# Performance work log

Hardware: AMD Instinct MI355X
Metric: run time of the kernel (lower is better)

## Reference

```python
import jax, jax.numpy as jnp
import numpy as np

B, D, H, DM, O = 8192, 512, 1024, 2048, 256


def setup_inputs() -> dict:
    key = jax.random.key(0)
    ks = jax.random.split(key, 24)
    def rn(k, shape, scale=1.0):
        return jax.random.normal(k, shape, dtype=jnp.float32) * scale
    w = 0.02  # weight init scale
    return {
        "x":  rn(ks[0], (B, D)),
        "h0": rn(ks[1], (B, H), 0.1), "h1": rn(ks[2], (B, H), 0.1),
        "c0": rn(ks[3], (B, H), 0.1), "c1": rn(ks[4], (B, H), 0.1),
        # Bernoulli keep masks with model_prob=1.0 -> all ones
        "m0": jnp.ones((B, H), jnp.float32), "m1": jnp.ones((B, H), jnp.float32),
        # layer 0 gate weights: in = D + H = 1536
        "Wf0": rn(ks[5], (D + H, H), w), "bf0": jnp.full((H,), 0.01, jnp.float32),
        "Wi0": rn(ks[6], (D + H, H), w), "bi0": jnp.full((H,), 0.01, jnp.float32),
        "Wc0": rn(ks[7], (D + H, H), w), "bc0": jnp.full((H,), 0.01, jnp.float32),
        "Wo0": rn(ks[8], (D + H, H), w), "bo0": jnp.full((H,), 0.01, jnp.float32),
        # layer 1 gate weights: in = H + H = 2048
        "Wf1": rn(ks[9],  (2 * H, H), w), "bf1": jnp.full((H,), 0.01, jnp.float32),
        "Wi1": rn(ks[10], (2 * H, H), w), "bi1": jnp.full((H,), 0.01, jnp.float32),
        "Wc1": rn(ks[11], (2 * H, H), w), "bc1": jnp.full((H,), 0.01, jnp.float32),
        "Wo1": rn(ks[12], (2 * H, H), w), "bo1": jnp.full((H,), 0.01, jnp.float32),
        # output MLP: H -> DM -> O (identity activation per default nn.Sequential())
        "Wm1": rn(ks[13], (H, DM), w), "bm1": jnp.full((DM,), 0.01, jnp.float32),
        "Wm2": rn(ks[14], (DM, O), w), "bm2": jnp.full((O,), 0.01, jnp.float32),
    }


def _lstm_cell(comb, c, Wf, bf, Wi, bi, Wc, bc, Wo, bo):
    # fuse the 4 gate GEMMs into one matmul, then split
    W = jnp.concatenate([Wf, Wi, Wc, Wo], axis=1)      # [in, 4H]
    b = jnp.concatenate([bf, bi, bc, bo])               # [4H]
    g = comb @ W + b                                    # [B, 4H]
    f, i, ct, o = jnp.split(g, 4, axis=1)
    c_new = jax.nn.sigmoid(f) * c + jax.nn.sigmoid(i) * jnp.tanh(ct)
    h_new = jax.nn.sigmoid(o) * jnp.tanh(c_new)
    return h_new, c_new


def reference(x, h0, h1, c0, c1, m0, m1,
              Wf0, bf0, Wi0, bi0, Wc0, bc0, Wo0, bo0,
              Wf1, bf1, Wi1, bi1, Wc1, bc1, Wo1, bo1,
              Wm1, bm1, Wm2, bm2):
    # layer 0: combined = cat(input, h0 * mask0)
    comb0 = jnp.concatenate([x, h0 * m0], axis=1)       # [B, D+H]
    h0n, c0n = _lstm_cell(comb0, c0, Wf0, bf0, Wi0, bi0, Wc0, bc0, Wo0, bo0)
    # layer 1: combined = cat(h0_new * mask0, h1 * mask1)
    comb1 = jnp.concatenate([h0n * m0, h1 * m1], axis=1)  # [B, 2H]
    h1n, c1n = _lstm_cell(comb1, c1, Wf1, bf1, Wi1, bi1, Wc1, bc1, Wo1, bo1)
    # output MLP (dropout p=0 is identity; activation is identity Sequential)
    out = (h1n @ Wm1 + bm1) @ Wm2 + bm2                 # [B, O]
    return out, h0n, h1n, c0n, c1n
```

## Files before the change

### kernel.cpp

```cpp
#include <hip/hip_runtime.h>
#include <hip/hip_bf16.h>
#include <cstdint>
#include <cstddef>

#define DI __device__ __forceinline__

typedef __attribute__((ext_vector_type(8))) short short8;
typedef __attribute__((ext_vector_type(4))) float f32x4;

static constexpr int Bb = 8192, Dd = 512, Hh = 1024;

DI short f2b(float f) {
  union { __hip_bfloat16 h; short s; } u;
  u.h = __float2bfloat16(f);
  return u.s;
}

DI float sigm(float x) {
  float e = __builtin_amdgcn_exp2f(-1.4426950408889634f * x);
  return __builtin_amdgcn_rcpf(1.0f + e);
}
DI float tanh_(float x) {
  float xc = fminf(fmaxf(x, -20.0f), 20.0f);
  float e = __builtin_amdgcn_exp2f(-2.8853900817779268f * xc);
  return (1.0f - e) * __builtin_amdgcn_rcpf(1.0f + e);
}

DI void gload16(const void* g, void* l) {
  __builtin_amdgcn_global_load_lds(
      (const __attribute__((address_space(1))) uint32_t*)g,
      (__attribute__((address_space(3))) uint32_t*)l, 16, 0, 0);
}


__global__ void conv_A0(const float* __restrict__ x, const float* __restrict__ h0,
                        const float* __restrict__ m0, short* __restrict__ A0) {
  const int row = blockIdx.x, t = threadIdx.x;
  float v[8];
  if (t < 64) {
    const float4* p = (const float4*)(x + (size_t)row * Dd + t * 8);
    float4 a = p[0], b = p[1];
    v[0] = a.x; v[1] = a.y; v[2] = a.z; v[3] = a.w;
    v[4] = b.x; v[5] = b.y; v[6] = b.z; v[7] = b.w;
  } else {
    const int j = t * 8 - 512;
    const float4* ph = (const float4*)(h0 + (size_t)row * Hh + j);
    const float4* pm = (const float4*)(m0 + (size_t)row * Hh + j);
    float4 a = ph[0], b = ph[1], ma = pm[0], mb = pm[1];
    v[0] = a.x * ma.x; v[1] = a.y * ma.y; v[2] = a.z * ma.z; v[3] = a.w * ma.w;
    v[4] = b.x * mb.x; v[5] = b.y * mb.y; v[6] = b.z * mb.z; v[7] = b.w * mb.w;
  }
  short8 o;
  #pragma unroll
  for (int q = 0; q < 8; q++) o[q] = f2b(v[q]);
  *(short8*)(A0 + (size_t)row * 1536 + t * 8) = o;
}

__global__ void conv_A1hi(const float* __restrict__ h1, const float* __restrict__ m1,
                          short* __restrict__ A1) {
  const int row = blockIdx.x, t = threadIdx.x;
  const int j = t * 8;
  const float4* ph = (const float4*)(h1 + (size_t)row * Hh + j);
  const float4* pm = (const float4*)(m1 + (size_t)row * Hh + j);
  float4 a = ph[0], b = ph[1], ma = pm[0], mb = pm[1];
  float v[8] = {a.x * ma.x, a.y * ma.y, a.z * ma.z, a.w * ma.w,
                b.x * mb.x, b.y * mb.y, b.z * mb.z, b.w * mb.w};
  short8 o;
  #pragma unroll
  for (int q = 0; q < 8; q++) o[q] = f2b(v[q]);
  *(short8*)(A1 + (size_t)row * 2048 + 1024 + j) = o;
}

__global__ void transpose_conv4(const float* __restrict__ s0, const float* __restrict__ s1,
                                const float* __restrict__ s2, const float* __restrict__ s3,
                                short* __restrict__ dst, int N, int K) {
  __shared__ float t[64][65];
  const int g = blockIdx.z;
  const float* src = (g == 0) ? s0 : (g == 1) ? s1 : (g == 2) ? s2 : s3;
  const int k0 = blockIdx.x * 64, n0 = blockIdx.y * 64;
  const int tid = threadIdx.x;
  const int r = tid >> 2, c0 = (tid & 3) * 16;
  const float* s = src + (size_t)(k0 + r) * N + n0 + c0;
  #pragma unroll
  for (int q = 0; q < 16; q += 4) {
    float4 v = *(const float4*)(s + q);
    t[r][c0 + q + 0] = v.x; t[r][c0 + q + 1] = v.y;
    t[r][c0 + q + 2] = v.z; t[r][c0 + q + 3] = v.w;
  }
  __syncthreads();
  const int n = n0 + r;
  const int j = (n >> 4) * 64 + g * 16 + (n & 15);
  short8 o0, o1;
  #pragma unroll
  for (int q = 0; q < 8; q++) o0[q] = f2b(t[c0 + q][r]);
  #pragma unroll
  for (int q = 0; q < 8; q++) o1[q] = f2b(t[c0 + 8 + q][r]);
  short* d = dst + (size_t)j * K + k0 + c0;
  *(short8*)d = o0;
  *((short8*)d + 1) = o1;
}

__global__ void transpose_conv(const float* __restrict__ src, short* __restrict__ dst,
                               int N, int K) {
  __shared__ float t[64][65];
  const int k0 = blockIdx.x * 64, n0 = blockIdx.y * 64;
  const int tid = threadIdx.x;
  const int r = tid >> 2, c0 = (tid & 3) * 16;
  const float* s = src + (size_t)(k0 + r) * N + n0 + c0;
  #pragma unroll
  for (int q = 0; q < 16; q += 4) {
    float4 v = *(const float4*)(s + q);
    t[r][c0 + q + 0] = v.x; t[r][c0 + q + 1] = v.y;
    t[r][c0 + q + 2] = v.z; t[r][c0 + q + 3] = v.w;
  }
  __syncthreads();
  const int n = n0 + r;
  short8 o0, o1;
  #pragma unroll
  for (int q = 0; q < 8; q++) o0[q] = f2b(t[c0 + q][r]);
  #pragma unroll
  for (int q = 0; q < 8; q++) o1[q] = f2b(t[c0 + 8 + q][r]);
  short* d = dst + (size_t)n * K + k0 + c0;
  *(short8*)d = o0;
  *((short8*)d + 1) = o1;
}

__global__ void conv_plain(const float* __restrict__ src, short* __restrict__ dst, int n8) {
  const int id = blockIdx.x * blockDim.x + threadIdx.x;
  if (id >= n8) return;
  const float4* p = (const float4*)(src + (size_t)id * 8);
  float4 a = p[0], b = p[1];
  short8 o;
  o[0] = f2b(a.x); o[1] = f2b(a.y); o[2] = f2b(a.z); o[3] = f2b(a.w);
  o[4] = f2b(b.x); o[5] = f2b(b.y); o[6] = f2b(b.z); o[7] = f2b(b.w);
  *(short8*)(dst + (size_t)id * 8) = o;
}

__global__ void bp_init(const float* __restrict__ bm2, float* __restrict__ bp) {
  bp[threadIdx.x] = bm2[threadIdx.x];
}
__global__ void bp_acc(const float* __restrict__ bm1, const float* __restrict__ Wm2,
                       float* __restrict__ bp) {
  const int o = threadIdx.x;
  const int k0 = blockIdx.x * 64;
  float s = 0.f;
  #pragma unroll 4
  for (int k = 0; k < 64; k++) s += bm1[k0 + k] * Wm2[(size_t)(k0 + k) * 256 + o];
  atomicAdd(&bp[o], s);
}

template <int EPI>
__global__ __launch_bounds__(256) void gemm_bt(
    const short* __restrict__ A, const short* __restrict__ Bt, int K,
    short* __restrict__ Cb, int ldc,
    float* __restrict__ outp, const float* __restrict__ bpv) {
  __shared__ __align__(16) short sA[128 * 32];
  __shared__ __align__(16) short sB[128 * 32];
  const int tid = threadIdx.x;
  const int lane = tid & 63;
  const int wave = tid >> 6;
  const int wm = wave >> 1, wn = wave & 1;
  const int bm = blockIdx.x, bn = blockIdx.y;
  const int lr = lane & 15, lq = lane >> 4;

  f32x4 acc[4][4] = {};

  const short* pA = A + ((size_t)(bm * 128 + (tid >> 2))) * K + (tid & 3) * 8;
  const short* pB = Bt + ((size_t)(bn * 128 + (tid >> 2))) * K + (tid & 3) * 8;
  short* lA = sA + tid * 8;
  short* lB = sB + tid * 8;
  const int aoff = (wm * 64 + lr) * 32 + lq * 8;
  const int boff = (wn * 64 + lr) * 32 + lq * 8;

  for (int k0 = 0; k0 < K; k0 += 32) {
    gload16(pA + k0, lA);
    gload16(pA + (size_t)64 * K + k0, lA + 2048);
    gload16(pB + k0, lB);
    gload16(pB + (size_t)64 * K + k0, lB + 2048);
    __syncthreads();
    short8 af[4], bv[4];
    #pragma unroll
    for (int m = 0; m < 4; m++) af[m] = *(const short8*)&sA[aoff + m * 512];
    #pragma unroll
    for (int n = 0; n < 4; n++) bv[n] = *(const short8*)&sB[boff + n * 512];
    #pragma unroll
    for (int m = 0; m < 4; m++)
      #pragma unroll
      for (int n = 0; n < 4; n++)
        acc[m][n] = __builtin_amdgcn_mfma_f32_16x16x32_bf16(af[m], bv[n], acc[m][n], 0, 0, 0);
    __syncthreads();
  }

  const int crow0 = bm * 128 + wm * 64 + lq * 4;
  const int ccol0 = bn * 128 + wn * 64 + lr;

  if constexpr (EPI == 0) {
    #pragma unroll
    for (int m = 0; m < 4; m++)
      #pragma unroll
      for (int r = 0; r < 4; r++) {
        const int row = crow0 + m * 16 + r;
        #pragma unroll
        for (int n = 0; n < 4; n++)
          Cb[(size_t)row * ldc + ccol0 + n * 16] = f2b(acc[m][n][r]);
      }
  } else {
    float bvv[4];
    #pragma unroll
    for (int n = 0; n < 4; n++) bvv[n] = bpv[ccol0 + n * 16];
    #pragma unroll
    for (int m = 0; m < 4; m++)
      #pragma unroll
      for (int r = 0; r < 4; r++) {
        const int row = crow0 + m * 16 + r;
        #pragma unroll
        for (int n = 0; n < 4; n++)
          outp[(size_t)row * 256 + ccol0 + n * 16] = acc[m][n][r] + bvv[n];
      }
  }
}


#define STA(buf, h, kt) { const short* s_ = gA + (size_t)(h) * 64 * K + (size_t)(kt) * 64; \
    gload16(s_ + aS0, &sA[buf][h][tid * 8]);                                               \
    gload16(s_ + aS1, &sA[buf][h][4096 + tid * 8]); }
#define STB(buf, h, kt) { const short* s_ = gB + (size_t)(h) * 128 * K + (size_t)(kt) * 64; \
    gload16(s_ + bS0, &sB[buf][h][tid * 8]);                                                \
    gload16(s_ + bS1, &sB[buf][h][4096 + tid * 8]); }

#define LDB(buf) {                                                \
    const short* bb = &sB[buf][bh][brb];                          \
    _Pragma("unroll") for (int n = 0; n < 4; n++) {               \
      bv[n][0] = *(const short8*)(bb + n * 1024 + sw0);           \
      bv[n][1] = *(const short8*)(bb + n * 1024 + sw1); } }

#define LDA_(buf, q, av) {                                        \
    const short* ab = &sA[buf][(q) >> 1][arb + ((q) & 1) * 2048]; \
    av[0][0] = *(const short8*)(ab + sw0);                        \
    av[0][1] = *(const short8*)(ab + sw1);                        \
    av[1][0] = *(const short8*)(ab + 1024 + sw0);                 \
    av[1][1] = *(const short8*)(ab + 1024 + sw1); }

#define MM(q, av) {                                               \
    __builtin_amdgcn_s_setprio(1);                                \
    _Pragma("unroll") for (int m = 0; m < 2; m++)                 \
    _Pragma("unroll") for (int n = 0; n < 4; n++) {               \
      acc[2*(q)+m][n] = __builtin_amdgcn_mfma_f32_16x16x32_bf16(av[m][0], bv[n][0], acc[2*(q)+m][n], 0, 0, 0); \
      acc[2*(q)+m][n] = __builtin_amdgcn_mfma_f32_16x16x32_bf16(av[m][1], bv[n][1], acc[2*(q)+m][n], 0, 0, 0); } \
    __builtin_amdgcn_s_setprio(0); }

#define BAR() asm volatile("s_barrier" ::: "memory")
#define VM6() asm volatile("s_waitcnt vmcnt(6)" ::: "memory")

#define PH(buf, q, STG, vm) { short8 av[2][2]; LDA_(buf, q, av); STG; \
    if (vm) VM6(); BAR(); MM(q, av); BAR(); }

__global__ __launch_bounds__(512, 2) void gemm8_lstm(
    const short* __restrict__ A, const short* __restrict__ Bt, const int K,
    const float* __restrict__ cprev, float* __restrict__ hout,
    float* __restrict__ cout, short* __restrict__ anext, const int ldan,
    const float* __restrict__ mask,
    const float* __restrict__ bF, const float* __restrict__ bI,
    const float* __restrict__ bC, const float* __restrict__ bO) {
  __shared__ __align__(16) short sA[2][2][8192];
  __shared__ __align__(16) short sB[2][2][8192];
  const int tid = threadIdx.x;
  const int lane = tid & 63, wid = tid >> 6;
  const int wr = wid >> 2, wc = wid & 3;
  const int lr = lane & 15, lq = lane >> 4;

  const int bm = blockIdx.x, bn = blockIdx.y;

  const int NT = K >> 6;
  const int NIT = NT >> 1;

  const int r0 = tid >> 3;
  const int csw = (tid & 7) ^ (r0 & 7);
  const int growA0 = ((r0 >> 5) & 1) * 32 + (r0 & 31);
  const int growA1 = 128 + growA0;
  const size_t aS0 = (size_t)growA0 * K + csw * 8;
  const size_t aS1 = (size_t)growA1 * K + csw * 8;
  const size_t bS0 = (size_t)r0 * K + csw * 8;
  const size_t bS1 = (size_t)(r0 + 64) * K + csw * 8;
  const short* gA = A + (size_t)bm * 256 * K;
  const short* gB = Bt + (size_t)bn * 256 * K;

  const int arb = (wr * 64 + lr) * 64;
  const int brb = ((wc & 1) * 64 + lr) * 64;
  const int bh = wc >> 1;
  const int sw0 = ((lq) ^ (lr & 7)) * 8;
  const int sw1 = ((4 + lq) ^ (lr & 7)) * 8;

  f32x4 acc[8][4] = {};
  short8 bv[4][2];

  STB(0, 0, 0); STB(0, 1, 0); STA(0, 0, 0); STA(0, 1, 0);
  STB(1, 0, 1); STB(1, 1, 1); STA(1, 0, 1);
  VM6(); BAR();

  for (int it = 0; it < NIT; ++it) {
    const int k1 = 2 * it + 1;
    int t2 = 2 * it + 2; if (t2 >= NT) t2 = 0;
    int t3 = 2 * it + 3; if (t3 >= NT) t3 = 1;
    { short8 av[2][2]; LDB(0); LDA_(0, 0, av); STA(1, 1, k1); BAR(); MM(0, av); BAR(); }
    PH(0, 1, STB(0, 0, t2), 0);
    PH(0, 2, STB(0, 1, t2), 0);
    PH(0, 3, STA(0, 0, t2), 1);
    { short8 av[2][2]; LDB(1); LDA_(1, 0, av); STA(0, 1, t2); BAR(); MM(0, av); BAR(); }
    PH(1, 1, STB(1, 0, t3), 0);
    PH(1, 2, STB(1, 1, t3), 0);
    PH(1, 3, STA(1, 0, t3), 1);
  }

  const int n = (bn * 4 + wc) * 16 + lr;
  const float bf_ = bF[n], bi_ = bI[n], bc_ = bC[n], bo_ = bO[n];
  const int row0 = bm * 256 + wr * 128 + lq * 4;

  float cp[4], mk[4], cpn[4], mkn[4];
  #pragma unroll
  for (int rr = 0; rr < 4; rr++) {
    const size_t idx = (size_t)(row0 + rr) * 1024 + n;
    cp[rr] = cprev[idx];
    mk[rr] = mask ? mask[idx] : 1.0f;
  }
  #pragma unroll
  for (int mf = 0; mf < 8; mf++) {
    if (mf < 7) {
      #pragma unroll
      for (int rr = 0; rr < 4; rr++) {
        const size_t idx2 = (size_t)(row0 + (mf + 1) * 16 + rr) * 1024 + n;
        cpn[rr] = cprev[idx2];
        mkn[rr] = mask ? mask[idx2] : 1.0f;
      }
    }
    #pragma unroll
    for (int rr = 0; rr < 4; rr++) {
      const int row = row0 + mf * 16 + rr;
      const size_t idx = (size_t)row * 1024 + n;
      const float fg = sigm(acc[mf][0][rr] + bf_);
      const float ig = sigm(acc[mf][1][rr] + bi_);
      const float cg = tanh_(acc[mf][2][rr] + bc_);
      const float og = sigm(acc[mf][3][rr] + bo_);
      const float cn = fg * cp[rr] + ig * cg;
      const float hn = og * tanh_(cn);
      cout[idx] = cn;
      hout[idx] = hn;
      anext[(size_t)row * ldan + n] = f2b(hn * mk[rr]);
    }
    #pragma unroll
    for (int rr = 0; rr < 4; rr++) { cp[rr] = cpn[rr]; mk[rr] = mkn[rr]; }
  }
}


extern "C" void kernel_launch(void* const* d_in, const int* in_sizes, int n_in,
                              void* d_out, int out_size, void* d_ws, size_t ws_size,
                              hipStream_t stream) {
  (void)in_sizes; (void)n_in; (void)out_size; (void)ws_size;
  const float* x   = (const float*)d_in[0];
  const float* h0  = (const float*)d_in[1];
  const float* h1  = (const float*)d_in[2];
  const float* c0  = (const float*)d_in[3];
  const float* c1  = (const float*)d_in[4];
  const float* m0  = (const float*)d_in[5];
  const float* m1  = (const float*)d_in[6];
  const float* Wf0 = (const float*)d_in[7];  const float* bf0 = (const float*)d_in[8];
  const float* Wi0 = (const float*)d_in[9];  const float* bi0 = (const float*)d_in[10];
  const float* Wc0 = (const float*)d_in[11]; const float* bc0 = (const float*)d_in[12];
  const float* Wo0 = (const float*)d_in[13]; const float* bo0 = (const float*)d_in[14];
  const float* Wf1 = (const float*)d_in[15]; const float* bf1 = (const float*)d_in[16];
  const float* Wi1 = (const float*)d_in[17]; const float* bi1 = (const float*)d_in[18];
  const float* Wc1 = (const float*)d_in[19]; const float* bc1 = (const float*)d_in[20];
  const float* Wo1 = (const float*)d_in[21]; const float* bo1 = (const float*)d_in[22];
  const float* Wm1 = (const float*)d_in[23]; const float* bm1 = (const float*)d_in[24];
  const float* Wm2 = (const float*)d_in[25]; const float* bm2 = (const float*)d_in[26];

  float* dout  = (float*)d_out;
  float* out_o = dout;
  float* h0n   = dout + 2097152;
  float* h1n   = h0n + 8388608;
  float* c0n   = h1n + 8388608;
  float* c1n   = c0n + 8388608;

  char* ws = (char*)d_ws;
  short* A0   = (short*)(ws);
  short* A1   = (short*)(ws + 25165824);
  short* A2   = (short*)(ws + 58720256);
  short* WT0  = (short*)(ws + 75497472);
  short* WT1  = (short*)(ws + 88080384);
  short* Wm1b = (short*)(ws + 104857600);
  short* Wm2T = (short*)(ws + 109051904);
  short* WpT  = (short*)(ws + 110100480);
  float* bp   = (float*)(ws + 110624768);

  conv_A0<<<dim3(8192), dim3(192), 0, stream>>>(x, h0, m0, A0);
  conv_A1hi<<<dim3(8192), dim3(128), 0, stream>>>(h1, m1, A1);
  transpose_conv4<<<dim3(24, 16, 4), dim3(256), 0, stream>>>(Wf0, Wi0, Wc0, Wo0, WT0, 1024, 1536);
  transpose_conv4<<<dim3(32, 16, 4), dim3(256), 0, stream>>>(Wf1, Wi1, Wc1, Wo1, WT1, 1024, 2048);
  conv_plain<<<dim3(1024), dim3(256), 0, stream>>>(Wm1, Wm1b, 262144);
  transpose_conv<<<dim3(32, 4), dim3(256), 0, stream>>>(Wm2, Wm2T, 256, 2048);
  bp_init<<<dim3(1), dim3(256), 0, stream>>>(bm2, bp);
  bp_acc<<<dim3(32), dim3(256), 0, stream>>>(bm1, Wm2, bp);

  gemm_bt<0><<<dim3(2, 8), dim3(256), 0, stream>>>(
      Wm2T, Wm1b, 2048, WpT, 1024, nullptr, nullptr);

  gemm8_lstm<<<dim3(32, 16), dim3(512), 0, stream>>>(
      A0, WT0, 1536, c0, h0n, c0n, A1, 2048, m0, bf0, bi0, bc0, bo0);

  gemm8_lstm<<<dim3(32, 16), dim3(512), 0, stream>>>(
      A1, WT1, 2048, c1, h1n, c1n, A2, 1024, nullptr, bf1, bi1, bc1, bo1);

  gemm_bt<1><<<dim3(64, 2), dim3(256), 0, stream>>>(
      A2, WpT, 1024, nullptr, 0, out_o, bp);
}
```

Before: 392.5 us.

## Shrink LSTM GEMM tile from 256x256 to 128x128 with more blocks

Replaces the 256x256 output tile per 512-thread block with a 128x128 tile. The grid grows from 32x16 to 64x32, LDS per block is halved, and launch bounds ask for 4 blocks per CU instead of 2. The warp layout changes to 4x2 with 2x4 MFMA fragments per wave, and the prefetch schedule is simplified to fit. The aim is higher occupancy and more parallel blocks to hide latency, at the cost of lower arithmetic intensity and more global/L2 traffic per FLOP.

```diff
diff --git a/kernel.cpp b/kernel.cpp
--- a/kernel.cpp
+++ b/kernel.cpp
@@ -221,54 +221,45 @@
 }
 
 
-#define STA(buf, h, kt) { const short* s_ = gA + (size_t)(h) * 64 * K + (size_t)(kt) * 64; \
-    gload16(s_ + aS0, &sA[buf][h][tid * 8]);                                               \
-    gload16(s_ + aS1, &sA[buf][h][4096 + tid * 8]); }
-#define STB(buf, h, kt) { const short* s_ = gB + (size_t)(h) * 128 * K + (size_t)(kt) * 64; \
-    gload16(s_ + bS0, &sB[buf][h][tid * 8]);                                                \
-    gload16(s_ + bS1, &sB[buf][h][4096 + tid * 8]); }
+#define STA(buf, h, kt) gload16(gA + (size_t)(h) * 64 * K + (size_t)(kt) * 64 + rofs, \
+                                &sA[buf][h][tid * 8])
+#define STB(buf, h, kt) gload16(gB + (size_t)(h) * 64 * K + (size_t)(kt) * 64 + rofs, \
+                                &sB[buf][h][tid * 8])
 
 #define LDB(buf) {                                                \
-    const short* bb = &sB[buf][bh][brb];                          \
+    const short* bb = &sB[buf][wn][lr * 64];                      \
     _Pragma("unroll") for (int n = 0; n < 4; n++) {               \
       bv[n][0] = *(const short8*)(bb + n * 1024 + sw0);           \
       bv[n][1] = *(const short8*)(bb + n * 1024 + sw1); } }
 
-#define LDA_(buf, q, av) {                                        \
-    const short* ab = &sA[buf][(q) >> 1][arb + ((q) & 1) * 2048]; \
-    av[0][0] = *(const short8*)(ab + sw0);                        \
-    av[0][1] = *(const short8*)(ab + sw1);                        \
-    av[1][0] = *(const short8*)(ab + 1024 + sw0);                 \
-    av[1][1] = *(const short8*)(ab + 1024 + sw1); }
-
-#define MM(q, av) {                                               \
+#define LDA_(buf, mf, av) {                                       \
+    const short* ab = &sA[buf][wm >> 1][((wm & 1) * 32 + (mf) * 16 + lr) * 64]; \
+    av[0] = *(const short8*)(ab + sw0);                           \
+    av[1] = *(const short8*)(ab + sw1); }
+
+#define MM(mf, av) {                                              \
     __builtin_amdgcn_s_setprio(1);                                \
-    _Pragma("unroll") for (int m = 0; m < 2; m++)                 \
     _Pragma("unroll") for (int n = 0; n < 4; n++) {               \
-      acc[2*(q)+m][n] = __builtin_amdgcn_mfma_f32_16x16x32_bf16(av[m][0], bv[n][0], acc[2*(q)+m][n], 0, 0, 0); \
-      acc[2*(q)+m][n] = __builtin_amdgcn_mfma_f32_16x16x32_bf16(av[m][1], bv[n][1], acc[2*(q)+m][n], 0, 0, 0); } \
+      acc[mf][n] = __builtin_amdgcn_mfma_f32_16x16x32_bf16(av[0], bv[n][0], acc[mf][n], 0, 0, 0); \
+      acc[mf][n] = __builtin_amdgcn_mfma_f32_16x16x32_bf16(av[1], bv[n][1], acc[mf][n], 0, 0, 0); } \
     __builtin_amdgcn_s_setprio(0); }
 
 #define BAR() asm volatile("s_barrier" ::: "memory")
-#define VM6() asm volatile("s_waitcnt vmcnt(6)" ::: "memory")
-
-#define PH(buf, q, STG, vm) { short8 av[2][2]; LDA_(buf, q, av); STG; \
-    if (vm) VM6(); BAR(); MM(q, av); BAR(); }
-
-__global__ __launch_bounds__(512, 2) void gemm8_lstm(
+#define VM2() asm volatile("s_waitcnt vmcnt(2)" ::: "memory")
+
+__global__ __launch_bounds__(512, 4) void gemm4_lstm(
     const short* __restrict__ A, const short* __restrict__ Bt, const int K,
     const float* __restrict__ cprev, float* __restrict__ hout,
     float* __restrict__ cout, short* __restrict__ anext, const int ldan,
     const float* __restrict__ mask,
     const float* __restrict__ bF, const float* __restrict__ bI,
     const float* __restrict__ bC, const float* __restrict__ bO) {
-  __shared__ __align__(16) short sA[2][2][8192];
-  __shared__ __align__(16) short sB[2][2][8192];
+  __shared__ __align__(16) short sA[2][2][4096];
+  __shared__ __align__(16) short sB[2][2][4096];
   const int tid = threadIdx.x;
   const int lane = tid & 63, wid = tid >> 6;
-  const int wr = wid >> 2, wc = wid & 3;
+  const int wm = wid >> 1, wn = wid & 1;
   const int lr = lane & 15, lq = lane >> 4;
-
   const int bm = blockIdx.x, bn = blockIdx.y;
 
   const int NT = K >> 6;
@@ -276,63 +267,49 @@
 
   const int r0 = tid >> 3;
   const int csw = (tid & 7) ^ (r0 & 7);
-  const int growA0 = ((r0 >> 5) & 1) * 32 + (r0 & 31);
-  const int growA1 = 128 + growA0;
-  const size_t aS0 = (size_t)growA0 * K + csw * 8;
-  const size_t aS1 = (size_t)growA1 * K + csw * 8;
-  const size_t bS0 = (size_t)r0 * K + csw * 8;
-  const size_t bS1 = (size_t)(r0 + 64) * K + csw * 8;
-  const short* gA = A + (size_t)bm * 256 * K;
-  const short* gB = Bt + (size_t)bn * 256 * K;
-
-  const int arb = (wr * 64 + lr) * 64;
-  const int brb = ((wc & 1) * 64 + lr) * 64;
-  const int bh = wc >> 1;
+  const size_t rofs = (size_t)r0 * K + csw * 8;
+  const short* gA = A + (size_t)bm * 128 * K;
+  const short* gB = Bt + (size_t)bn * 128 * K;
+
   const int sw0 = ((lq) ^ (lr & 7)) * 8;
   const int sw1 = ((4 + lq) ^ (lr & 7)) * 8;
 
-  f32x4 acc[8][4] = {};
+  f32x4 acc[2][4] = {};
   short8 bv[4][2];
 
   STB(0, 0, 0); STB(0, 1, 0); STA(0, 0, 0); STA(0, 1, 0);
-  STB(1, 0, 1); STB(1, 1, 1); STA(1, 0, 1);
-  VM6(); BAR();
+  STB(1, 0, 1); STB(1, 1, 1);
+  VM2(); BAR();
 
   for (int it = 0; it < NIT; ++it) {
     const int k1 = 2 * it + 1;
     int t2 = 2 * it + 2; if (t2 >= NT) t2 = 0;
     int t3 = 2 * it + 3; if (t3 >= NT) t3 = 1;
-    { short8 av[2][2]; LDB(0); LDA_(0, 0, av); STA(1, 1, k1); BAR(); MM(0, av); BAR(); }
-    PH(0, 1, STB(0, 0, t2), 0);
-    PH(0, 2, STB(0, 1, t2), 0);
-    PH(0, 3, STA(0, 0, t2), 1);
-    { short8 av[2][2]; LDB(1); LDA_(1, 0, av); STA(0, 1, t2); BAR(); MM(0, av); BAR(); }
-    PH(1, 1, STB(1, 0, t3), 0);
-    PH(1, 2, STB(1, 1, t3), 0);
-    PH(1, 3, STA(1, 0, t3), 1);
-  }
-
-  const int n = (bn * 4 + wc) * 16 + lr;
+    { short8 av[2]; LDB(0); LDA_(0, 0, av); STA(1, 0, k1); STA(1, 1, k1);
+      BAR(); MM(0, av); BAR(); }
+    { short8 av[2]; LDA_(0, 1, av); STB(0, 0, t2); STB(0, 1, t2);
+      VM2(); BAR(); MM(1, av); BAR(); }
+    { short8 av[2]; LDB(1); LDA_(1, 0, av); STA(0, 0, t2); STA(0, 1, t2);
+      BAR(); MM(0, av); BAR(); }
+    { short8 av[2]; LDA_(1, 1, av); STB(1, 0, t3); STB(1, 1, t3);
+      VM2(); BAR(); MM(1, av); BAR(); }
+  }
+
+  const int n = bn * 32 + wn * 16 + lr;
   const float bf_ = bF[n], bi_ = bI[n], bc_ = bC[n], bo_ = bO[n];
-  const int row0 = bm * 256 + wr * 128 + lq * 4;
-
-  float cp[4], mk[4], cpn[4], mkn[4];
-  #pragma unroll
-  for (int rr = 0; rr < 4; rr++) {
-    const size_t idx = (size_t)(row0 + rr) * 1024 + n;
-    cp[rr] = cprev[idx];
-    mk[rr] = mask ? mask[idx] : 1.0f;
-  }
-  #pragma unroll
-  for (int mf = 0; mf < 8; mf++) {
-    if (mf < 7) {
-      #pragma unroll
-      for (int rr = 0; rr < 4; rr++) {
-        const size_t idx2 = (size_t)(row0 + (mf + 1) * 16 + rr) * 1024 + n;
-        cpn[rr] = cprev[idx2];
-        mkn[rr] = mask ? mask[idx2] : 1.0f;
-      }
+  const int row0 = bm * 128 + wm * 32 + lq * 4;
+
+  float cp[2][4], mk[2][4];
+  #pragma unroll
+  for (int mf = 0; mf < 2; mf++)
+    #pragma unroll
+    for (int rr = 0; rr < 4; rr++) {
+      const size_t idx = (size_t)(row0 + mf * 16 + rr) * 1024 + n;
+      cp[mf][rr] = cprev[idx];
+      mk[mf][rr] = mask ? mask[idx] : 1.0f;
     }
+  #pragma unroll
+  for (int mf = 0; mf < 2; mf++) {
     #pragma unroll
     for (int rr = 0; rr < 4; rr++) {
       const int row = row0 + mf * 16 + rr;
@@ -341,14 +318,12 @@
       const float ig = sigm(acc[mf][1][rr] + bi_);
       const float cg = tanh_(acc[mf][2][rr] + bc_);
       const float og = sigm(acc[mf][3][rr] + bo_);
-      const float cn = fg * cp[rr] + ig * cg;
+      const float cn = fg * cp[mf][rr] + ig * cg;
       const float hn = og * tanh_(cn);
       cout[idx] = cn;
       hout[idx] = hn;
-      anext[(size_t)row * ldan + n] = f2b(hn * mk[rr]);
+      anext[(size_t)row * ldan + n] = f2b(hn * mk[mf][rr]);
     }
-    #pragma unroll
-    for (int rr = 0; rr < 4; rr++) { cp[rr] = cpn[rr]; mk[rr] = mkn[rr]; }
   }
 }
 
@@ -405,10 +380,10 @@
   gemm_bt<0><<<dim3(2, 8), dim3(256), 0, stream>>>(
       Wm2T, Wm1b, 2048, WpT, 1024, nullptr, nullptr);
 
-  gemm8_lstm<<<dim3(32, 16), dim3(512), 0, stream>>>(
+  gemm4_lstm<<<dim3(64, 32), dim3(512), 0, stream>>>(
       A0, WT0, 1536, c0, h0n, c0n, A1, 2048, m0, bf0, bi0, bc0, bo0);
 
-  gemm8_lstm<<<dim3(32, 16), dim3(512), 0, stream>>>(
+  gemm4_lstm<<<dim3(64, 32), dim3(512), 0, stream>>>(
       A1, WT1, 2048, c1, h1n, c1n, A2, 1024, nullptr, bf1, bi1, bc1, bo1);
 
   gemm_bt<1><<<dim3(64, 2), dim3(256), 0, stream>>>(
```

New measurement: 405.1 us. +3.2%, slower.

## Split LSTM gate GEMM across 16 waves per block instead of 8

Applied to the files above, without the earlier changes.

Reworks the fused LSTM gate GEMM kernel to launch 1024 threads (16 waves) per 256x256 tile instead of 512. Each wave now owns 64 rows instead of 128, so it holds half the accumulators, and the global-to-LDS staging needs one 16-byte load per thread per half-tile. The wait count, the per-wave A-fragment addressing and the epilogue row mapping are changed to match. The aim is more latency hiding and lower register pressure per wave, at the cost of more barrier participants and B-fragment LDS reads repeated across twice as many waves.

```diff
diff --git a/kernel.cpp b/kernel.cpp
--- a/kernel.cpp
+++ b/kernel.cpp
@@ -221,41 +221,33 @@
 }
 
 
-#define STA(buf, h, kt) { const short* s_ = gA + (size_t)(h) * 64 * K + (size_t)(kt) * 64; \
-    gload16(s_ + aS0, &sA[buf][h][tid * 8]);                                               \
-    gload16(s_ + aS1, &sA[buf][h][4096 + tid * 8]); }
-#define STB(buf, h, kt) { const short* s_ = gB + (size_t)(h) * 128 * K + (size_t)(kt) * 64; \
-    gload16(s_ + bS0, &sB[buf][h][tid * 8]);                                                \
-    gload16(s_ + bS1, &sB[buf][h][4096 + tid * 8]); }
+#define STA(buf, h, kt) gload16(gA + (size_t)(h) * 128 * K + (size_t)(kt) * 64 + rofs, \
+                                &sA[buf][h][tid * 8])
+#define STB(buf, h, kt) gload16(gB + (size_t)(h) * 128 * K + (size_t)(kt) * 64 + rofs, \
+                                &sB[buf][h][tid * 8])
 
 #define LDB(buf) {                                                \
-    const short* bb = &sB[buf][bh][brb];                          \
+    const short* bb = &sB[buf][wc >> 1][((wc & 1) * 64 + lr) * 64]; \
     _Pragma("unroll") for (int n = 0; n < 4; n++) {               \
       bv[n][0] = *(const short8*)(bb + n * 1024 + sw0);           \
       bv[n][1] = *(const short8*)(bb + n * 1024 + sw1); } }
 
 #define LDA_(buf, q, av) {                                        \
-    const short* ab = &sA[buf][(q) >> 1][arb + ((q) & 1) * 2048]; \
-    av[0][0] = *(const short8*)(ab + sw0);                        \
-    av[0][1] = *(const short8*)(ab + sw1);                        \
-    av[1][0] = *(const short8*)(ab + 1024 + sw0);                 \
-    av[1][1] = *(const short8*)(ab + 1024 + sw1); }
+    const short* ab = &sA[buf][(q) >> 1][(((q) & 1) * 64 + wr * 16 + lr) * 64]; \
+    av[0] = *(const short8*)(ab + sw0);                           \
+    av[1] = *(const short8*)(ab + sw1); }
 
 #define MM(q, av) {                                               \
     __builtin_amdgcn_s_setprio(1);                                \
-    _Pragma("unroll") for (int m = 0; m < 2; m++)                 \
     _Pragma("unroll") for (int n = 0; n < 4; n++) {               \
-      acc[2*(q)+m][n] = __builtin_amdgcn_mfma_f32_16x16x32_bf16(av[m][0], bv[n][0], acc[2*(q)+m][n], 0, 0, 0); \
-      acc[2*(q)+m][n] = __builtin_amdgcn_mfma_f32_16x16x32_bf16(av[m][1], bv[n][1], acc[2*(q)+m][n], 0, 0, 0); } \
+      acc[q][n] = __builtin_amdgcn_mfma_f32_16x16x32_bf16(av[0], bv[n][0], acc[q][n], 0, 0, 0); \
+      acc[q][n] = __builtin_amdgcn_mfma_f32_16x16x32_bf16(av[1], bv[n][1], acc[q][n], 0, 0, 0); } \
     __builtin_amdgcn_s_setprio(0); }
 
 #define BAR() asm volatile("s_barrier" ::: "memory")
-#define VM6() asm volatile("s_waitcnt vmcnt(6)" ::: "memory")
-
-#define PH(buf, q, STG, vm) { short8 av[2][2]; LDA_(buf, q, av); STG; \
-    if (vm) VM6(); BAR(); MM(q, av); BAR(); }
-
-__global__ __launch_bounds__(512, 2) void gemm8_lstm(
+#define VM3() asm volatile("s_waitcnt vmcnt(3)" ::: "memory")
+
+__global__ __launch_bounds__(1024, 4) void gemm16_lstm(
     const short* __restrict__ A, const short* __restrict__ Bt, const int K,
     const float* __restrict__ cprev, float* __restrict__ hout,
     float* __restrict__ cout, short* __restrict__ anext, const int ldan,
@@ -268,7 +260,6 @@
   const int lane = tid & 63, wid = tid >> 6;
   const int wr = wid >> 2, wc = wid & 3;
   const int lr = lane & 15, lq = lane >> 4;
-
   const int bm = blockIdx.x, bn = blockIdx.y;
 
   const int NT = K >> 6;
@@ -276,45 +267,37 @@
 
   const int r0 = tid >> 3;
   const int csw = (tid & 7) ^ (r0 & 7);
-  const int growA0 = ((r0 >> 5) & 1) * 32 + (r0 & 31);
-  const int growA1 = 128 + growA0;
-  const size_t aS0 = (size_t)growA0 * K + csw * 8;
-  const size_t aS1 = (size_t)growA1 * K + csw * 8;
-  const size_t bS0 = (size_t)r0 * K + csw * 8;
-  const size_t bS1 = (size_t)(r0 + 64) * K + csw * 8;
+  const size_t rofs = (size_t)r0 * K + csw * 8;
   const short* gA = A + (size_t)bm * 256 * K;
   const short* gB = Bt + (size_t)bn * 256 * K;
 
-  const int arb = (wr * 64 + lr) * 64;
-  const int brb = ((wc & 1) * 64 + lr) * 64;
-  const int bh = wc >> 1;
   const int sw0 = ((lq) ^ (lr & 7)) * 8;
   const int sw1 = ((4 + lq) ^ (lr & 7)) * 8;
 
-  f32x4 acc[8][4] = {};
+  f32x4 acc[4][4] = {};
   short8 bv[4][2];
 
-  STB(0, 0, 0); STB(0, 1, 0); STA(0, 0, 0); STA(0, 1, 0);
-  STB(1, 0, 1); STB(1, 1, 1); STA(1, 0, 1);
-  VM6(); BAR();
+  STB(0, 0, 0); STA(0, 0, 0); STB(0, 1, 0); STA(0, 1, 0);
+  STB(1, 0, 1); STA(1, 0, 1); STB(1, 1, 1);
+  VM3(); BAR();
 
   for (int it = 0; it < NIT; ++it) {
     const int k1 = 2 * it + 1;
     int t2 = 2 * it + 2; if (t2 >= NT) t2 = 0;
     int t3 = 2 * it + 3; if (t3 >= NT) t3 = 1;
-    { short8 av[2][2]; LDB(0); LDA_(0, 0, av); STA(1, 1, k1); BAR(); MM(0, av); BAR(); }
-    PH(0, 1, STB(0, 0, t2), 0);
-    PH(0, 2, STB(0, 1, t2), 0);
-    PH(0, 3, STA(0, 0, t2), 1);
-    { short8 av[2][2]; LDB(1); LDA_(1, 0, av); STA(0, 1, t2); BAR(); MM(0, av); BAR(); }
-    PH(1, 1, STB(1, 0, t3), 0);
-    PH(1, 2, STB(1, 1, t3), 0);
-    PH(1, 3, STA(1, 0, t3), 1);
+    { short8 av[2]; LDB(0); LDA_(0, 0, av); STA(1, 1, k1); BAR(); MM(0, av); BAR(); }
+    { short8 av[2]; LDA_(0, 1, av); STB(0, 0, t2); BAR(); MM(1, av); BAR(); }
+    { short8 av[2]; LDA_(0, 2, av); STA(0, 0, t2); BAR(); MM(2, av); BAR(); }
+    { short8 av[2]; LDA_(0, 3, av); STB(0, 1, t2); VM3(); BAR(); MM(3, av); BAR(); }
+    { short8 av[2]; LDB(1); LDA_(1, 0, av); STA(0, 1, t2); BAR(); MM(0, av); BAR(); }
+    { short8 av[2]; LDA_(1, 1, av); STB(1, 0, t3); BAR(); MM(1, av); BAR(); }
+    { short8 av[2]; LDA_(1, 2, av); STA(1, 0, t3); BAR(); MM(2, av); BAR(); }
+    { short8 av[2]; LDA_(1, 3, av); STB(1, 1, t3); VM3(); BAR(); MM(3, av); BAR(); }
   }
 
   const int n = (bn * 4 + wc) * 16 + lr;
   const float bf_ = bF[n], bi_ = bI[n], bc_ = bC[n], bo_ = bO[n];
-  const int row0 = bm * 256 + wr * 128 + lq * 4;
+  const int row0 = bm * 256 + wr * 16 + lq * 4;
 
   float cp[4], mk[4], cpn[4], mkn[4];
   #pragma unroll
@@ -324,23 +307,23 @@
     mk[rr] = mask ? mask[idx] : 1.0f;
   }
   #pragma unroll
-  for (int mf = 0; mf < 8; mf++) {
-    if (mf < 7) {
+  for (int q = 0; q < 4; q++) {
+    if (q < 3) {
       #pragma unroll
       for (int rr = 0; rr < 4; rr++) {
-        const size_t idx2 = (size_t)(row0 + (mf + 1) * 16 + rr) * 1024 + n;
+        const size_t idx2 = (size_t)(row0 + (q + 1) * 64 + rr) * 1024 + n;
         cpn[rr] = cprev[idx2];
         mkn[rr] = mask ? mask[idx2] : 1.0f;
       }
     }
     #pragma unroll
     for (int rr = 0; rr < 4; rr++) {
-      const int row = row0 + mf * 16 + rr;
+      const int row = row0 + q * 64 + rr;
       const size_t idx = (size_t)row * 1024 + n;
-      const float fg = sigm(acc[mf][0][rr] + bf_);
-      const float ig = sigm(acc[mf][1][rr] + bi_);
-      const float cg = tanh_(acc[mf][2][rr] + bc_);
-      const float og = sigm(acc[mf][3][rr] + bo_);
+      const float fg = sigm(acc[q][0][rr] + bf_);
+      const float ig = sigm(acc[q][1][rr] + bi_);
+      const float cg = tanh_(acc[q][2][rr] + bc_);
+      const float og = sigm(acc[q][3][rr] + bo_);
       const float cn = fg * cp[rr] + ig * cg;
       const float hn = og * tanh_(cn);
       cout[idx] = cn;
@@ -405,10 +388,10 @@
   gemm_bt<0><<<dim3(2, 8), dim3(256), 0, stream>>>(
       Wm2T, Wm1b, 2048, WpT, 1024, nullptr, nullptr);
 
-  gemm8_lstm<<<dim3(32, 16), dim3(512), 0, stream>>>(
+  gemm16_lstm<<<dim3(32, 16), dim3(1024), 0, stream>>>(
       A0, WT0, 1536, c0, h0n, c0n, A1, 2048, m0, bf0, bi0, bc0, bo0);
 
-  gemm8_lstm<<<dim3(32, 16), dim3(512), 0, stream>>>(
+  gemm16_lstm<<<dim3(32, 16), dim3(1024), 0, stream>>>(
       A1, WT1, 2048, c1, h1n, c1n, A2, 1024, nullptr, bf1, bi1, bc1, bo1);
 
   gemm_bt<1><<<dim3(64, 2), dim3(256), 0, stream>>>(
```

Result: no change. 399.6 us (+1.8%).

## Double-buffer LDS fragment registers to overlap shared loads with MFMA

Applied to the files above, without the earlier changes.

The LSTM gate GEMM main loop now loads the next A/B LDS fragments into a second register set before issuing the MFMAs on the current set. This software-pipelines LDS reads against matrix math instead of waiting on them each phase. The vmcnt waits are retuned to match the new stage order. It raises register pressure, which under launch bounds of 512 threads and 2 blocks could cause spills, and it changes the barrier/waitcnt ordering, which carries correctness risk.

```diff
diff --git a/kernel.cpp b/kernel.cpp
--- a/kernel.cpp
+++ b/kernel.cpp
@@ -228,20 +228,20 @@
     gload16(s_ + bS0, &sB[buf][h][tid * 8]);                                                \
     gload16(s_ + bS1, &sB[buf][h][4096 + tid * 8]); }
 
-#define LDB(buf) {                                                \
+#define LDBv(buf, bv) {                                           \
     const short* bb = &sB[buf][bh][brb];                          \
     _Pragma("unroll") for (int n = 0; n < 4; n++) {               \
       bv[n][0] = *(const short8*)(bb + n * 1024 + sw0);           \
       bv[n][1] = *(const short8*)(bb + n * 1024 + sw1); } }
 
-#define LDA_(buf, q, av) {                                        \
+#define LDAv(buf, q, av) {                                        \
     const short* ab = &sA[buf][(q) >> 1][arb + ((q) & 1) * 2048]; \
     av[0][0] = *(const short8*)(ab + sw0);                        \
     av[0][1] = *(const short8*)(ab + sw1);                        \
     av[1][0] = *(const short8*)(ab + 1024 + sw0);                 \
     av[1][1] = *(const short8*)(ab + 1024 + sw1); }
 
-#define MM(q, av) {                                               \
+#define MM2(q, av, bv) {                                          \
     __builtin_amdgcn_s_setprio(1);                                \
     _Pragma("unroll") for (int m = 0; m < 2; m++)                 \
     _Pragma("unroll") for (int n = 0; n < 4; n++) {               \
@@ -250,12 +250,9 @@
     __builtin_amdgcn_s_setprio(0); }
 
 #define BAR() asm volatile("s_barrier" ::: "memory")
-#define VM6() asm volatile("s_waitcnt vmcnt(6)" ::: "memory")
-
-#define PH(buf, q, STG, vm) { short8 av[2][2]; LDA_(buf, q, av); STG; \
-    if (vm) VM6(); BAR(); MM(q, av); BAR(); }
-
-__global__ __launch_bounds__(512, 2) void gemm8_lstm(
+#define VMW(n) asm volatile("s_waitcnt vmcnt(" #n ")" ::: "memory")
+
+__global__ __launch_bounds__(512, 2) void gemm8p_lstm(
     const short* __restrict__ A, const short* __restrict__ Bt, const int K,
     const float* __restrict__ cprev, float* __restrict__ hout,
     float* __restrict__ cout, short* __restrict__ anext, const int ldan,
@@ -268,7 +265,6 @@
   const int lane = tid & 63, wid = tid >> 6;
   const int wr = wid >> 2, wc = wid & 3;
   const int lr = lane & 15, lq = lane >> 4;
-
   const int bm = blockIdx.x, bn = blockIdx.y;
 
   const int NT = K >> 6;
@@ -292,24 +288,26 @@
   const int sw1 = ((4 + lq) ^ (lr & 7)) * 8;
 
   f32x4 acc[8][4] = {};
-  short8 bv[4][2];
+  short8 bv0[4][2], bv1[4][2];
+  short8 av_a[2][2], av_b[2][2];
 
   STB(0, 0, 0); STB(0, 1, 0); STA(0, 0, 0); STA(0, 1, 0);
   STB(1, 0, 1); STB(1, 1, 1); STA(1, 0, 1);
-  VM6(); BAR();
+  VMW(6); BAR();
+  LDBv(0, bv0); LDAv(0, 0, av_a);
 
   for (int it = 0; it < NIT; ++it) {
     const int k1 = 2 * it + 1;
     int t2 = 2 * it + 2; if (t2 >= NT) t2 = 0;
     int t3 = 2 * it + 3; if (t3 >= NT) t3 = 1;
-    { short8 av[2][2]; LDB(0); LDA_(0, 0, av); STA(1, 1, k1); BAR(); MM(0, av); BAR(); }
-    PH(0, 1, STB(0, 0, t2), 0);
-    PH(0, 2, STB(0, 1, t2), 0);
-    PH(0, 3, STA(0, 0, t2), 1);
-    { short8 av[2][2]; LDB(1); LDA_(1, 0, av); STA(0, 1, t2); BAR(); MM(0, av); BAR(); }
-    PH(1, 1, STB(1, 0, t3), 0);
-    PH(1, 2, STB(1, 1, t3), 0);
-    PH(1, 3, STA(1, 0, t3), 1);
+    LDAv(0, 1, av_b); STA(1, 1, k1); BAR(); MM2(0, av_a, bv0); VMW(8); BAR();
+    LDAv(0, 2, av_a); STB(0, 0, t2); BAR(); MM2(1, av_b, bv0); BAR();
+    LDAv(0, 3, av_b); STB(0, 1, t2); BAR(); MM2(2, av_a, bv0); VMW(6); BAR();
+    LDBv(1, bv1); LDAv(1, 0, av_a); STA(0, 0, t2); BAR(); MM2(3, av_b, bv0); BAR();
+    LDAv(1, 1, av_b); STA(0, 1, t2); BAR(); MM2(0, av_a, bv1); VMW(8); BAR();
+    LDAv(1, 2, av_a); STB(1, 0, t3); BAR(); MM2(1, av_b, bv1); BAR();
+    LDAv(1, 3, av_b); STB(1, 1, t3); BAR(); MM2(2, av_a, bv1); VMW(6); BAR();
+    LDBv(0, bv0); LDAv(0, 0, av_a); STA(1, 0, t3); BAR(); MM2(3, av_b, bv1); BAR();
   }
 
   const int n = (bn * 4 + wc) * 16 + lr;
@@ -405,10 +403,10 @@
   gemm_bt<0><<<dim3(2, 8), dim3(256), 0, stream>>>(
       Wm2T, Wm1b, 2048, WpT, 1024, nullptr, nullptr);
 
-  gemm8_lstm<<<dim3(32, 16), dim3(512), 0, stream>>>(
+  gemm8p_lstm<<<dim3(32, 16), dim3(512), 0, stream>>>(
       A0, WT0, 1536, c0, h0n, c0n, A1, 2048, m0, bf0, bi0, bc0, bo0);
 
-  gemm8_lstm<<<dim3(32, 16), dim3(512), 0, stream>>>(
+  gemm8p_lstm<<<dim3(32, 16), dim3(512), 0, stream>>>(
       A1, WT1, 2048, c1, h1n, c1n, A2, 1024, nullptr, bf1, bi1, bc1, bo1);
 
   gemm_bt<1><<<dim3(64, 2), dim3(256), 0, stream>>>(
```

Result: slower. 420.8 us (median of 2 runs) (+7.2%).
